# Optimization experiments

Hardware: AMD Instinct MI355X
Metric: run time of the kernel (lower is better)

The kernel has to match this reference:

```python
import jax, jax.numpy as jnp
import numpy as np

B, DIM, HEADS, H, W = 4, 64, 8, 512, 512


def _conv(x, w, groups=1):
    # NCHW x, OIHW w, stride 1, SAME padding (padding=k//2 in torch)
    return jax.lax.conv_general_dilated(
        x, w, (1, 1), 'SAME', feature_group_count=groups,
        dimension_numbers=('NCHW', 'OIHW', 'NCHW'))


def _dwt_haar(x):
    # single-level orthonormal haar on even-sized NCHW input
    a = x[..., 0::2, 0::2]; b = x[..., 0::2, 1::2]
    c = x[..., 1::2, 0::2]; d = x[..., 1::2, 1::2]
    LL = (a + b + c + d) * 0.5
    LH = (-a - b + c + d) * 0.5
    HL = (-a + b - c + d) * 0.5
    HH = (a - b - c + d) * 0.5
    return LL, LH, HL, HH


def _idwt_haar(LL, LH, HL, HH):
    a = (LL - LH - HL + HH) * 0.5
    b = (LL - LH + HL - HH) * 0.5
    c = (LL + LH - HL - HH) * 0.5
    d = (LL + LH + HL + HH) * 0.5
    Bn, C, h, w = LL.shape
    even = jnp.stack([a, b], -1).reshape(Bn, C, h, 2 * w)  # rows 0::2
    odd = jnp.stack([c, d], -1).reshape(Bn, C, h, 2 * w)   # rows 1::2
    return jnp.stack([even, odd], -2).reshape(Bn, C, 2 * h, 2 * w)


def _l2norm(x, eps=1e-12):
    n = jnp.sqrt(jnp.sum(x * x, axis=-1, keepdims=True))
    return x / jnp.maximum(n, eps)


def setup_inputs() -> dict:
    key = jax.random.key(0)
    ks = jax.random.split(key, 8)
    def w(k, shape):
        fan_in = shape[1] * shape[2] * shape[3]
        return jax.random.normal(k, shape, jnp.float32) * (1.0 / np.sqrt(fan_in))
    return {
        'x': jax.random.normal(ks[0], (B, DIM, H, W), jnp.float32),
        'w_hc1': w(ks[1], (2 * DIM, DIM, 3, 3)),        # groups=2 over 2*dim channels
        'w_hc2': w(ks[2], (DIM, 2 * DIM, 1, 1)),
        'w_ho': w(ks[3], (3 * DIM, DIM, 3, 3)),          # groups=3 over 3*dim channels
        'w_qkv': w(ks[4], (3 * DIM, DIM, 1, 1)),
        'w_dw': w(ks[5], (3 * DIM, 1, 3, 3)),            # depthwise, groups=3*dim
        'w_proj': w(ks[6], (DIM, DIM, 1, 1)),
        'temperature': jnp.ones((HEADS, 1, 1), jnp.float32),
    }


def reference(x, w_hc1, w_hc2, w_ho, w_qkv, w_dw, w_proj, temperature):
    LL, LH, HL, HH = _dwt_haar(x)

    # high-frequency (LH,HL) filter branch
    hv = jnp.concatenate([LH, HL], axis=1)
    filter_hv = jax.nn.relu(_conv(jax.nn.relu(_conv(hv, w_hc1, groups=2)), w_hc2))

    # qkv from LL: 1x1 conv then depthwise 3x3
    qkv = _conv(_conv(LL, w_qkv), w_dw, groups=3 * DIM)
    q, k, v = jnp.split(qkv, 3, axis=1)
    b, c, h, w = q.shape
    v = v * filter_hv + v

    ch = c // HEADS
    q = q.reshape(b, HEADS, ch, h * w)
    k = k.reshape(b, HEADS, ch, h * w)
    v = v.reshape(b, HEADS, ch, h * w)
    q = _l2norm(q)
    k = _l2norm(k)

    attn = jnp.einsum('bhcn,bhdn->bhcd', q, k) * temperature  # [b,heads,ch,ch]
    attn = jax.nn.softmax(attn, axis=-1)
    out = jnp.einsum('bhcd,bhdn->bhcn', attn, v).reshape(b, c, h, w)
    out = _conv(out, w_proj)

    # high-frequency output branch
    yh = jax.nn.relu(_conv(jnp.concatenate([LH, HL, HH], axis=1), w_ho, groups=3))
    LH2, HL2, HH2 = jnp.split(yh, 3, axis=1)

    return _idwt_haar(out, LH2, HL2, HH2)
```

## Files before the change

### kernel.cpp

```cpp
#include <hip/hip_runtime.h>
#include <hip/hip_bf16.h>

#define BN 4
#define DIM 64
#define NHEADS 8
#define HH 256
#define WH 256
#define NP (HH*WH)
#define HF 512
#define WF 512

#define PD 258
#define PROW (PD*64)
#define PPLANE ((size_t)PD*PD*64)

typedef __attribute__((ext_vector_type(8))) short bfx8;
typedef __attribute__((ext_vector_type(8))) unsigned short u16x8;
typedef __attribute__((ext_vector_type(4))) unsigned short u16x4;
typedef __attribute__((ext_vector_type(4))) float f32x4;

static __device__ __forceinline__ short f2bf(float f) {
    unsigned u = __float_as_uint(f);
    unsigned r = (u + 0x7FFFu + ((u >> 16) & 1u)) >> 16;
    return (short)r;
}
static __device__ __forceinline__ float bfu(unsigned short u) {
    return __uint_as_float((unsigned)u << 16);
}

__global__ __launch_bounds__(256) void k_setup(unsigned short* __restrict__ tiled16,
                                               const float* __restrict__ w_ho,
                                               const float* __restrict__ w_hc1,
                                               const float* __restrict__ w_hc2,
                                               const float* __restrict__ w_qkv,
                                               short* __restrict__ wrHO,
                                               short* __restrict__ wrHC1,
                                               short* __restrict__ wrHC2,
                                               short* __restrict__ wrQKV) {
    int bx = blockIdx.x, tid = threadIdx.x;
    if (bx < 16) {
        char* base = (char*)(tiled16 + (size_t)bx * PPLANE);
        const int ROWB = PROW * 2;
        for (int k = tid; k < 8224; k += 256) {
            char* dst;
            if (k < 2064) dst = base + (size_t)k * 16;
            else if (k < 4128) dst = base + (size_t)257 * ROWB + (size_t)(k - 2064) * 16;
            else if (k < 6176) { int r = (k - 4128) >> 3, s = (k - 4128) & 7;
                dst = base + (size_t)(r + 1) * ROWB + (size_t)s * 16; }
            else { int r = (k - 6176) >> 3, s = (k - 6176) & 7;
                dst = base + (size_t)(r + 1) * ROWB + 257 * 128 + (size_t)s * 16; }
            *(uint4*)dst = (uint4){0, 0, 0, 0};
        }
        return;
    }
    if (bx < 16 + 432 + 288) {
        const float* w = (bx < 448) ? w_ho : w_hc1;
        short* wrep = (bx < 448) ? wrHO : wrHC1;
        int t = (bx - ((bx < 448) ? 16 : 448)) * 256 + tid;
        unsigned g   = (unsigned)t / 36864u;
        unsigned r1  = (unsigned)t % 36864u;
        unsigned tap = r1 / 4096u;
        unsigned r2  = r1 % 4096u;
        unsigned icb = r2 / 512u;
        unsigned r3  = r2 % 512u;
        unsigned oc  = r3 >> 3;
        unsigned j   = r3 & 7u;
        wrep[t] = f2bf(w[(((size_t)g * 64 + oc) * 64 + icb * 8u + j) * 9 + tap]);
        return;
    }
    if (bx < 16 + 432 + 288 + 32) {
        int t = (bx - 736) * 256 + tid;
        int j = t & 7, gr = t >> 3, o16 = gr & 15, X = gr >> 4;
        int icb = X % 16, oct = X / 16;
        wrHC2[t] = f2bf(w_hc2[(size_t)(oct * 16 + o16) * 128 + icb * 8 + j]);
        return;
    }
    {
        int t = (bx - 768) * 256 + tid;
        int j = t & 7, gr = t >> 3, o16 = gr & 15, X = gr >> 4;
        int icb = X % 8, oct = X / 8;
        wrQKV[t] = f2bf(w_qkv[(size_t)(oct * 16 + o16) * 64 + icb * 8 + j]);
    }
}

__global__ __launch_bounds__(256) void k_dwt(const float* __restrict__ x,
                                             unsigned short* __restrict__ tiled,
                                             unsigned short* __restrict__ llp) {
    __shared__ unsigned short lds[3 * 128 * 64] __attribute__((aligned(16)));
    const int tid = threadIdx.x;
    const int pid = blockIdx.x;
    const int b = blockIdx.y;
    const int y0 = (pid >> 4) * 8, x0 = (pid & 15) * 16;
    const int quad = tid & 127;
    const int qy = quad >> 4, qx = quad & 15;
    const int gy = y0 + qy, gx = x0 + qx;
    const int ich = tid >> 7;
    unsigned short* llb = llp + (size_t)b * PPLANE + ((size_t)(gy + 1) * PD + (gx + 1)) * 64;

#pragma unroll 4
    for (int it = 0; it < 16; ++it) {
        int ic = it * 4 + ich * 2;
        unsigned g = (((unsigned)(ic >> 3)) + (unsigned)gx + 2u * (unsigned)gy) & 7u;
        unsigned swz = (unsigned)quad * 64 + (g << 3) + (unsigned)(ic & 7);
        unsigned pk[3], pll;
#pragma unroll
        for (int s = 0; s < 2; ++s) {
            const float* px = x + (((size_t)(b * 64 + ic + s) * HF) + 2 * gy) * WF + 2 * gx;
            float2 e0 = *(const float2*)px;
            float2 e1 = *(const float2*)(px + WF);
            float a = e0.x, bb = e0.y, c = e1.x, d = e1.y;
            unsigned ll = (unsigned short)f2bf(( a + bb + c + d) * 0.5f);
            unsigned lh = (unsigned short)f2bf((-a - bb + c + d) * 0.5f);
            unsigned hl = (unsigned short)f2bf((-a + bb - c + d) * 0.5f);
            unsigned hh = (unsigned short)f2bf(( a - bb - c + d) * 0.5f);
            if (s == 0) { pll = ll; pk[0] = lh; pk[1] = hl; pk[2] = hh; }
            else { pll |= ll << 16; pk[0] |= lh << 16; pk[1] |= hl << 16; pk[2] |= hh << 16; }
        }
        *(unsigned*)&lds[swz]          = pk[0];
        *(unsigned*)&lds[8192 + swz]   = pk[1];
        *(unsigned*)&lds[16384 + swz]  = pk[2];
        *(unsigned*)&llb[(g << 3) + (unsigned)(ic & 7)] = pll;
    }
    __syncthreads();
#pragma unroll
    for (int it = 0; it < 12; ++it) {
        int cch = tid + it * 256;
        int p = cch >> 10, rem = cch & 1023;
        int row = rem >> 7, col = rem & 127;
        unsigned short* dst = tiled + ((size_t)(b * 3 + p) * PD + (y0 + row + 1)) * PROW
                                    + (size_t)(x0 + 1) * 64 + (size_t)col * 8;
        *(uint4*)dst = *(const uint4*)((const char*)lds + (size_t)cch * 16);
    }
}

template <int LAYOUT>
__global__ __launch_bounds__(256) void k_gconv3x3_mfma(const unsigned short* __restrict__ tiled,
                                                       const bfx8* __restrict__ wr,
                                                       unsigned short* __restrict__ out, int OC) {
    __shared__ short lds_in[324 * 64] __attribute__((aligned(16)));
    const int tid = threadIdx.x;
    const int l = tid & 63, wv = tid >> 6;
    const int tile = blockIdx.x;
    const int x0 = (tile & 15) * 16, y0 = (tile >> 4) * 16;
    const int g = blockIdx.y, b = blockIdx.z;
    const unsigned short* src = tiled + (size_t)(b * 3 + g) * PPLANE;

#pragma unroll
    for (int it = 0; it < 10; ++it) {
        int cch = it * 256 + tid;
        unsigned row = (unsigned)cch / 144u, col = (unsigned)cch % 144u;
        const unsigned short* ga = src + (size_t)(y0 + row) * PROW + (size_t)x0 * 64 + (size_t)col * 8;
        __builtin_amdgcn_global_load_lds(
            (const __attribute__((address_space(1))) void*)ga,
            (__attribute__((address_space(3))) void*)((char*)lds_in + (size_t)(it * 256 + wv * 64) * 16),
            16, 0, 0);
    }
    if (tid < 32) {
        int cch = 2560 + tid;
        unsigned row = (unsigned)cch / 144u, col = (unsigned)cch % 144u;
        const unsigned short* ga = src + (size_t)(y0 + row) * PROW + (size_t)x0 * 64 + (size_t)col * 8;
        *(uint4*)((char*)lds_in + (size_t)cch * 16) = *(const uint4*)ga;
    }
    __syncthreads();

    f32x4 acc[4][4];
#pragma unroll
    for (int i = 0; i < 4; ++i)
#pragma unroll
        for (int j = 0; j < 4; ++j) acc[i][j] = (f32x4){0.f, 0.f, 0.f, 0.f};

    const int lx = l & 15, lq = l >> 4;
#pragma unroll
    for (int c = 0; c < 2; ++c) {
        const int icb = c * 4 + lq;
#pragma unroll
        for (int tap = 0; tap < 9; ++tap) {
            const int dy = tap / 3, dx = tap % 3;
            const size_t wbase = ((size_t)(g * 9 + tap) * 8 + icb) * 64 + lx;
            bfx8 b0 = wr[wbase];
            bfx8 b1 = wr[wbase + 16];
            bfx8 b2 = wr[wbase + 32];
            bfx8 b3 = wr[wbase + 48];
#pragma unroll
            for (int pg = 0; pg < 4; ++pg) {
                int hy = wv * 4 + pg + dy, hx = lx + dx;
                int hp = hy * 18 + hx;
                const bfx8* ap = (const bfx8*)&lds_in[hp * 64 + (((icb + hx + 2 * hy + 5) & 7) << 3)];
                bfx8 a = *ap;
                acc[pg][0] = __builtin_amdgcn_mfma_f32_16x16x32_bf16(a, b0, acc[pg][0], 0, 0, 0);
                acc[pg][1] = __builtin_amdgcn_mfma_f32_16x16x32_bf16(a, b1, acc[pg][1], 0, 0, 0);
                acc[pg][2] = __builtin_amdgcn_mfma_f32_16x16x32_bf16(a, b2, acc[pg][2], 0, 0, 0);
                acc[pg][3] = __builtin_amdgcn_mfma_f32_16x16x32_bf16(a, b3, acc[pg][3], 0, 0, 0);
            }
        }
    }

#pragma unroll
    for (int pg = 0; pg < 4; ++pg) {
#pragma unroll
        for (int ocg = 0; ocg < 4; ++ocg) {
            f32x4 v = acc[pg][ocg];
            if (LAYOUT == 0) {
                unsigned short* op = out + ((size_t)(b * 256 + tile) * OC + g * 64 + ocg * 16 + lx) * 256
                                         + (wv * 4 + pg) * 16 + lq * 4;
                ushort4 s4;
                s4.x = (unsigned short)f2bf(fmaxf(v.x, 0.f));
                s4.y = (unsigned short)f2bf(fmaxf(v.y, 0.f));
                s4.z = (unsigned short)f2bf(fmaxf(v.z, 0.f));
                s4.w = (unsigned short)f2bf(fmaxf(v.w, 0.f));
                *(ushort4*)op = s4;
            } else {
                int icT = g * 64 + ocg * 16 + lx;
                int g16 = icT >> 3;
                unsigned short* tb = out + ((size_t)(b * 256 + tile) * 256) * 128;
                int innerb = (wv * 4 + pg) * 16 + lq * 4;
                float vr[4] = {v.x, v.y, v.z, v.w};
#pragma unroll
                for (int r = 0; r < 4; ++r) {
                    int inn = innerb + r;
                    tb[(size_t)inn * 128 + (((g16 + inn) & 15) << 3) + (icT & 7)] =
                        (unsigned short)f2bf(fmaxf(vr[r], 0.f));
                }
            }
        }
    }
}

template <int CIN, int OC, bool RELU>
__global__ __launch_bounds__(256) void k_conv1x1_mfma(const unsigned short* __restrict__ inT,
                                                      const bfx8* __restrict__ wr,
                                                      unsigned short* __restrict__ out) {
    constexpr int KB = CIN / 8;
    constexpr int KC = CIN / 32;
    constexpr int NOCT = OC / 16;
    __shared__ short ldsA[256 * CIN] __attribute__((aligned(16)));
    const int tid = threadIdx.x;
    const int l = tid & 63, wv = tid >> 6;
    const int tile = blockIdx.x, b = blockIdx.y;
    const unsigned short* src = inT + ((size_t)(b * 256 + tile) * 256) * CIN;
    constexpr int ITER = (256 * CIN / 8) / 256;
#pragma unroll
    for (int it = 0; it < ITER; ++it) {
        int cc = it * 256 + tid;
        __builtin_amdgcn_global_load_lds(
            (const __attribute__((address_space(1))) void*)(src + (size_t)cc * 8),
            (__attribute__((address_space(3))) void*)((char*)ldsA + (size_t)(it * 256 + wv * 64) * 16),
            16, 0, 0);
    }
    __syncthreads();

    const int lx = l & 15, lq = l >> 4;
#pragma unroll
    for (int o4 = 0; o4 < NOCT / 4; ++o4) {
        f32x4 acc[4][4];
#pragma unroll
        for (int i = 0; i < 4; ++i)
#pragma unroll
            for (int j = 0; j < 4; ++j) acc[i][j] = (f32x4){0.f, 0.f, 0.f, 0.f};
#pragma unroll
        for (int c = 0; c < KC; ++c) {
            const int icb = c * 4 + lq;
            bfx8 bf[4];
#pragma unroll
            for (int ot = 0; ot < 4; ++ot)
                bf[ot] = wr[(size_t)(((o4 * 4 + ot) * KB + icb) * 16) + lx];
#pragma unroll
            for (int pg = 0; pg < 4; ++pg) {
                int inner = (wv * 4 + pg) * 16 + lx;
                const bfx8* ap = (const bfx8*)&ldsA[inner * CIN + (((icb + inner) & (KB - 1)) << 3)];
                bfx8 a = *ap;
                acc[pg][0] = __builtin_amdgcn_mfma_f32_16x16x32_bf16(a, bf[0], acc[pg][0], 0, 0, 0);
                acc[pg][1] = __builtin_amdgcn_mfma_f32_16x16x32_bf16(a, bf[1], acc[pg][1], 0, 0, 0);
                acc[pg][2] = __builtin_amdgcn_mfma_f32_16x16x32_bf16(a, bf[2], acc[pg][2], 0, 0, 0);
                acc[pg][3] = __builtin_amdgcn_mfma_f32_16x16x32_bf16(a, bf[3], acc[pg][3], 0, 0, 0);
            }
        }
#pragma unroll
        for (int pg = 0; pg < 4; ++pg)
#pragma unroll
            for (int ot = 0; ot < 4; ++ot) {
                int oc = (o4 * 4 + ot) * 16 + lx;
                unsigned short* op = out + ((size_t)(b * 256 + tile) * OC + oc) * 256
                                         + (wv * 4 + pg) * 16 + lq * 4;
                f32x4 v = acc[pg][ot];
                ushort4 s4;
                s4.x = (unsigned short)f2bf(RELU ? fmaxf(v.x, 0.f) : v.x);
                s4.y = (unsigned short)f2bf(RELU ? fmaxf(v.y, 0.f) : v.y);
                s4.z = (unsigned short)f2bf(RELU ? fmaxf(v.z, 0.f) : v.z);
                s4.w = (unsigned short)f2bf(RELU ? fmaxf(v.w, 0.f) : v.w);
                *(ushort4*)op = s4;
            }
    }
}

__global__ __launch_bounds__(256) void k_qkv_fused(const unsigned short* __restrict__ llp,
                                                   const bfx8* __restrict__ wrq,
                                                   const float* __restrict__ wdw,
                                                   const unsigned short* __restrict__ filt,
                                                   unsigned short* __restrict__ vt,
                                                   float* __restrict__ praw,
                                                   float* __restrict__ praw2) {
    __shared__ short ldsA[336 * 64] __attribute__((aligned(16)));
    __shared__ short qsave[64 * 256] __attribute__((aligned(16)));
    __shared__ float ssq[2][4][64];
    const int tid = threadIdx.x;
    const int l = tid & 63, wv = tid >> 6;
    const int tile = blockIdx.x, b = blockIdx.y;
    const int x0 = (tile & 15) * 16, y0 = (tile >> 4) * 16;
    const unsigned short* src = llp + (size_t)b * PPLANE;

#pragma unroll
    for (int it = 0; it < 10; ++it) {
        int cch = it * 256 + tid;
        unsigned row = (unsigned)cch / 144u, col = (unsigned)cch % 144u;
        const unsigned short* ga = src + (size_t)(y0 + row) * PROW + (size_t)x0 * 64 + (size_t)col * 8;
        __builtin_amdgcn_global_load_lds(
            (const __attribute__((address_space(1))) void*)ga,
            (__attribute__((address_space(3))) void*)((char*)ldsA + (size_t)(it * 256 + wv * 64) * 16),
            16, 0, 0);
    }
    if (tid < 32) {
        int cch = 2560 + tid;
        unsigned row = (unsigned)cch / 144u, col = (unsigned)cch % 144u;
        const unsigned short* ga = src + (size_t)(y0 + row) * PROW + (size_t)x0 * 64 + (size_t)col * 8;
        *(uint4*)((char*)ldsA + (size_t)cch * 16) = *(const uint4*)ga;
    }
    __syncthreads();

    const int lx = l & 15, lq = l >> 4;
    bfx8 af[6][2];
#pragma unroll
    for (int m = 0; m < 6; ++m) {
        int mt = wv + 4 * m;
        if (mt < 21) {
            int hp = mt * 16 + lx;
            int hy = hp / 18, hx = hp - hy * 18;
#pragma unroll
            for (int kc = 0; kc < 2; ++kc) {
                int icb = kc * 4 + lq;
                af[m][kc] = *(const bfx8*)&ldsA[hp * 64 + (((icb + hx + 2 * hy + 5) & 7) << 3)];
            }
        }
    }
    __syncthreads();

    for (int g3 = 0; g3 < 3; ++g3) {
        bfx8 bw[2][4];
#pragma unroll
        for (int kc = 0; kc < 2; ++kc)
#pragma unroll
            for (int nt = 0; nt < 4; ++nt)
                bw[kc][nt] = wrq[(size_t)(((g3 * 4 + nt) * 8) + kc * 4 + lq) * 16 + lx];
#pragma unroll
        for (int m = 0; m < 6; ++m) {
            int mt = wv + 4 * m;
            if (mt < 21) {
                f32x4 acc[4];
#pragma unroll
                for (int nt = 0; nt < 4; ++nt) acc[nt] = (f32x4){0.f, 0.f, 0.f, 0.f};
#pragma unroll
                for (int kc = 0; kc < 2; ++kc) {
                    bfx8 a = af[m][kc];
#pragma unroll
                    for (int nt = 0; nt < 4; ++nt)
                        acc[nt] = __builtin_amdgcn_mfma_f32_16x16x32_bf16(a, bw[kc][nt], acc[nt], 0, 0, 0);
                }
#pragma unroll
                for (int nt = 0; nt < 4; ++nt) {
                    int ocl = nt * 16 + lx;
                    float vr[4] = {acc[nt].x, acc[nt].y, acc[nt].z, acc[nt].w};
#pragma unroll
                    for (int r = 0; r < 4; ++r) {
                        int hp2 = mt * 16 + lq * 4 + r;
                        int hy2 = hp2 / 18, hx2 = hp2 - hy2 * 18;
                        ldsA[hp2 * 64 + ((((ocl >> 3) + hx2 + 2 * hy2) & 7) << 3) + (ocl & 7)] =
                            f2bf(vr[r]);
                    }
                }
            }
        }
        __syncthreads();
        const int ch = l, chg = g3 * 64 + ch;
        float w9[9];
#pragma unroll
        for (int t = 0; t < 9; ++t) w9[t] = wdw[chg * 9 + t];
        float s2 = 0.f;
        u16x8 kpk[4][2];
#pragma unroll
        for (int yy = 0; yy < 4; ++yy) {
            int y = wv * 4 + yy;
            float ln[3][18];
#pragma unroll
            for (int hr = 0; hr < 3; ++hr) {
                int hy = y + hr;
#pragma unroll
                for (int hx = 0; hx < 18; ++hx)
                    ln[hr][hx] = bfu((unsigned short)ldsA[(hy * 18 + hx) * 64 +
                                     ((((ch >> 3) + hx + 2 * hy) & 7) << 3) + (ch & 7)]);
            }
            float ox[16];
#pragma unroll
            for (int xx = 0; xx < 16; ++xx) {
                float s = 0.f;
#pragma unroll
                for (int hr = 0; hr < 3; ++hr)
#pragma unroll
                    for (int dx = 0; dx < 3; ++dx)
                        s = fmaf(ln[hr][xx + dx], w9[hr * 3 + dx], s);
                ox[xx] = s;
            }
            if (g3 == 2) {
                const unsigned short* fp = filt + ((size_t)(b * 256 + tile) * 64 + ch) * 256 + y * 16;
                u16x8 f0 = *(const u16x8*)fp;
                u16x8 f1 = *(const u16x8*)(fp + 8);
#pragma unroll
                for (int k = 0; k < 8; ++k) ox[k]     = fmaf(ox[k],     bfu(f0[k]), ox[k]);
#pragma unroll
                for (int k = 0; k < 8; ++k) ox[8 + k] = fmaf(ox[8 + k], bfu(f1[k]), ox[8 + k]);
                unsigned short* vb = vt + ((size_t)(b * 256 + tile) * 256 + (size_t)y * 16) * 64 + ch;
#pragma unroll
                for (int xx = 0; xx < 16; ++xx) vb[xx * 64] = (unsigned short)f2bf(ox[xx]);
            } else {
#pragma unroll
                for (int xx = 0; xx < 16; ++xx) s2 = fmaf(ox[xx], ox[xx], s2);
                if (g3 == 0) {
#pragma unroll
                    for (int xx = 0; xx < 16; ++xx) {
                        int px = y * 16 + xx;
                        qsave[ch * 256 + ((((px >> 3) + ch) & 31) << 3) + (px & 7)] =
                            f2bf(ox[xx]);
                    }
                } else {
#pragma unroll
                    for (int xx = 0; xx < 8; ++xx)  kpk[yy][0][xx] = (unsigned short)f2bf(ox[xx]);
#pragma unroll
                    for (int xx = 0; xx < 8; ++xx)  kpk[yy][1][xx] = (unsigned short)f2bf(ox[8 + xx]);
                }
            }
        }
        if (g3 == 0) ssq[0][wv][ch] = s2;
        if (g3 == 1) {
            ssq[1][wv][ch] = s2;
            __syncthreads();
            short* kbuf = ldsA;
#pragma unroll
            for (int yy = 0; yy < 4; ++yy) {
                int y = wv * 4 + yy;
#pragma unroll
                for (int xx = 0; xx < 16; ++xx) {
                    int px = y * 16 + xx;
                    kbuf[ch * 256 + ((((px >> 3) + ch) & 31) << 3) + (px & 7)] =
                        (short)kpk[yy][xx >> 3][xx & 7];
                }
            }
            __syncthreads();
            f32x4 sacc[4];
#pragma unroll
            for (int t16 = 0; t16 < 4; ++t16) sacc[t16] = (f32x4){0.f, 0.f, 0.f, 0.f};
#pragma unroll
            for (int kc2 = 0; kc2 < 2; ++kc2) {
                int kc = wv * 2 + kc2;
#pragma unroll
                for (int t16 = 0; t16 < 4; ++t16) {
                    int chh = t16 * 16 + lx;
                    int go = chh * 256 + (((kc * 4 + lq + chh) & 31) << 3);
                    bfx8 aq = *(const bfx8*)&qsave[go];
                    bfx8 bk = *(const bfx8*)&kbuf[go];
                    sacc[t16] = __builtin_amdgcn_mfma_f32_16x16x32_bf16(aq, bk, sacc[t16], 0, 0, 0);
                }
            }
            __syncthreads();
            float* sred = (float*)qsave;
#pragma unroll
            for (int t16 = 0; t16 < 4; ++t16)
                *(f32x4*)&sred[((wv * 4 + t16) * 64 + l) * 4] = sacc[t16];
            __syncthreads();
            {
                int t16r = tid >> 6, lr = tid & 63;
                f32x4 s0 = *(const f32x4*)&sred[((0 * 4 + t16r) * 64 + lr) * 4];
                f32x4 s1 = *(const f32x4*)&sred[((1 * 4 + t16r) * 64 + lr) * 4];
                f32x4 s2r = *(const f32x4*)&sred[((2 * 4 + t16r) * 64 + lr) * 4];
                f32x4 s3 = *(const f32x4*)&sred[((3 * 4 + t16r) * 64 + lr) * 4];
                f32x4 sum = s0 + s1 + s2r + s3;
                *(f32x4*)&praw[(((size_t)(b * 256 + tile) * 4 + t16r) * 64 + lr) * 4] = sum;
                if (tid < 128) {
                    int which = tid >> 6, chh = tid & 63;
                    praw2[(size_t)(b * 256 + tile) * 128 + tid] =
                        ssq[which][0][chh] + ssq[which][1][chh] +
                        ssq[which][2][chh] + ssq[which][3][chh];
                }
            }
        }
        __syncthreads();
    }
}

__global__ __launch_bounds__(512) void k_soft_prep(const float* __restrict__ praw,
                                                   const float* __restrict__ praw2,
                                                   const float* __restrict__ temp,
                                                   const float* __restrict__ wproj,
                                                   short* __restrict__ mrep) {
    __shared__ float sm[512];
    __shared__ float ash[512];
    const int b = blockIdx.x, tid = threadIdx.x;
    const int hd = tid >> 6, t = tid & 63;
    const int c = t >> 3, d = t & 7;
    const int t16 = hd >> 1, half = hd & 1;
    const int cl = half * 8 + c, dl = half * 8 + d;
    const float* pb = praw + ((size_t)(b * 256) * 4 + t16) * 256 + ((cl >> 2) * 16 + dl) * 4 + (cl & 3);
    const float* p2 = praw2 + (size_t)(b * 256) * 128;
    float s = 0.f, sq = 0.f, sk = 0.f;
    for (int tile = 0; tile < 256; ++tile) {
        s  += pb[(size_t)tile * 1024];
        sq += p2[(size_t)tile * 128 + hd * 8 + c];
        sk += p2[(size_t)tile * 128 + 64 + hd * 8 + d];
    }
    float nq = fmaxf(sqrtf(sq), 1e-12f);
    float nk = fmaxf(sqrtf(sk), 1e-12f);
    s = s / (nq * nk) * temp[hd];
    sm[tid] = s;
    __syncthreads();
    float mx = -1e30f;
#pragma unroll
    for (int dd = 0; dd < 8; ++dd) mx = fmaxf(mx, sm[hd * 64 + c * 8 + dd]);
    float e = __expf(s - mx);
    ash[tid] = e;
    __syncthreads();
    float sum = 0.f;
#pragma unroll
    for (int dd = 0; dd < 8; ++dd) sum += ash[hd * 64 + c * 8 + dd];
    float a = e / sum;
    __syncthreads();
    ash[tid] = a;
    __syncthreads();
#pragma unroll
    for (int i = 0; i < 8; ++i) {
        int idx = tid * 8 + i;
        int j = idx & 7, o16 = (idx >> 3) & 15, icb = (idx >> 7) & 7, oct = idx >> 10;
        int oc = oct * 16 + o16;
        float m = 0.f;
#pragma unroll
        for (int c8 = 0; c8 < 8; ++c8)
            m = fmaf(wproj[(size_t)oc * 64 + icb * 8 + c8], ash[icb * 64 + c8 * 8 + j], m);
        mrep[(size_t)b * 4096 + idx] = f2bf(m);
    }
}

__global__ __launch_bounds__(256) void k_attnout_idwt(const unsigned short* __restrict__ vt,
                                                      const bfx8* __restrict__ mrep,
                                                      const unsigned short* __restrict__ yht,
                                                      float* __restrict__ out) {
    const int tid = threadIdx.x;
    const int l = tid & 63, wv = tid >> 6;
    const int lx = l & 15, lq = l >> 4;
    const int tile = blockIdx.x, b = blockIdx.y;
    const int x0 = (tile & 15) * 16, y0 = (tile >> 4) * 16;
    const bfx8* vtb = (const bfx8*)(vt + (size_t)(b * 256 + tile) * 256 * 64);
    const bfx8* mb = mrep + (size_t)b * 512;

    bfx8 bw[2][4];
#pragma unroll
    for (int kc = 0; kc < 2; ++kc)
#pragma unroll
        for (int nt = 0; nt < 4; ++nt)
            bw[kc][nt] = mb[(nt * 8 + kc * 4 + lq) * 16 + lx];

    const unsigned short* yb = yht + (size_t)(b * 256 + tile) * 192 * 256;

#pragma unroll
    for (int pg = 0; pg < 4; ++pg) {
        const int mt = wv * 4 + pg;
        const int y = y0 + mt;
        bfx8 a0 = vtb[(mt * 16 + lx) * 8 + lq];
        bfx8 a1 = vtb[(mt * 16 + lx) * 8 + 4 + lq];

        f32x4 acc[4];
#pragma unroll
        for (int nt = 0; nt < 4; ++nt) acc[nt] = (f32x4){0.f, 0.f, 0.f, 0.f};
#pragma unroll
        for (int nt = 0; nt < 4; ++nt) {
            acc[nt] = __builtin_amdgcn_mfma_f32_16x16x32_bf16(a0, bw[0][nt], acc[nt], 0, 0, 0);
            acc[nt] = __builtin_amdgcn_mfma_f32_16x16x32_bf16(a1, bw[1][nt], acc[nt], 0, 0, 0);
        }
#pragma unroll
        for (int nt = 0; nt < 4; ++nt) {
            const int oc = nt * 16 + lx;
            const int inner = mt * 16 + lq * 4;
            const unsigned short* yp = yb + (size_t)oc * 256 + inner;
            u16x4 lh4 = *(const u16x4*)yp;
            u16x4 hl4 = *(const u16x4*)(yp + (size_t)64 * 256);
            u16x4 hh4 = *(const u16x4*)(yp + (size_t)128 * 256);
            float e0[8], e1[8];
#pragma unroll
            for (int r = 0; r < 4; ++r) {
                float s  = acc[nt][r];
                float LH = bfu(lh4[r]), HL = bfu(hl4[r]), HHv = bfu(hh4[r]);
                e0[2 * r]     = (s - LH - HL + HHv) * 0.5f;
                e0[2 * r + 1] = (s - LH + HL - HHv) * 0.5f;
                e1[2 * r]     = (s + LH - HL - HHv) * 0.5f;
                e1[2 * r + 1] = (s + LH + HL + HHv) * 0.5f;
            }
            float* o0 = out + ((size_t)(b * 64 + oc) * HF + 2 * y) * WF + 2 * (x0 + lq * 4);
            *(float4*)o0            = *(float4*)&e0[0];
            *(float4*)(o0 + 4)      = *(float4*)&e0[4];
            *(float4*)(o0 + WF)     = *(float4*)&e1[0];
            *(float4*)(o0 + WF + 4) = *(float4*)&e1[4];
        }
    }
}

extern "C" void kernel_launch(void* const* d_in, const int* in_sizes, int n_in,
                              void* d_out, int out_size, void* d_ws, size_t ws_size,
                              hipStream_t stream) {
    const float* x      = (const float*)d_in[0];
    const float* w_hc1  = (const float*)d_in[1];
    const float* w_hc2  = (const float*)d_in[2];
    const float* w_ho   = (const float*)d_in[3];
    const float* w_qkv  = (const float*)d_in[4];
    const float* w_dw   = (const float*)d_in[5];
    const float* w_proj = (const float*)d_in[6];
    const float* temp   = (const float*)d_in[7];
    float* out = (float*)d_out;

    char* base = (char*)d_ws;
    unsigned short* TILED = (unsigned short*)(base + 0);
    unsigned short* LLP   = (unsigned short*)(base + 102242304ULL);
    unsigned short* YH    = (unsigned short*)(base + 136323072ULL);
    unsigned short* T1T   = (unsigned short*)(base + 236986368ULL);
    unsigned short* FILT  = (unsigned short*)(base + 304095232ULL);
    unsigned short* VT    = (unsigned short*)(base + 337649664ULL);
    float*          PRAW  = (float*)(base + 371204096ULL);
    float*          PRAW2 = (float*)(base + 375398400ULL);
    short* WREP_HO  = (short*)(base + 375922688ULL);
    short* WREP_HC1 = (short*)(base + 376143872ULL);
    short* WREP_HC2 = (short*)(base + 376291328ULL);
    short* WREP_QKV = (short*)(base + 376307712ULL);
    short* MREP     = (short*)(base + 376332288ULL);

    k_setup<<<816, 256, 0, stream>>>(TILED, w_ho, w_hc1, w_hc2, w_qkv,
                                     WREP_HO, WREP_HC1, WREP_HC2, WREP_QKV);
    k_dwt<<<dim3(512, BN), 256, 0, stream>>>(x, TILED, LLP);
    k_gconv3x3_mfma<0><<<dim3(256, 3, BN), 256, 0, stream>>>(TILED, (const bfx8*)WREP_HO, YH, 192);
    k_gconv3x3_mfma<1><<<dim3(256, 2, BN), 256, 0, stream>>>(TILED, (const bfx8*)WREP_HC1, T1T, 128);
    k_conv1x1_mfma<128, 64, true><<<dim3(256, BN), 256, 0, stream>>>(T1T, (const bfx8*)WREP_HC2, FILT);
    k_qkv_fused<<<dim3(256, BN), 256, 0, stream>>>(LLP, (const bfx8*)WREP_QKV, w_dw, FILT,
                                                   VT, PRAW, PRAW2);
    k_soft_prep<<<BN, 512, 0, stream>>>(PRAW, PRAW2, temp, w_proj, MREP);
    k_attnout_idwt<<<dim3(256, BN), 256, 0, stream>>>(VT, (const bfx8*)MREP, YH, out);
}
```

Measured before the change: 559.2 us.

## Halve qkv tile height to 8 rows to cut LDS and raise occupancy

The fused qkv kernel now processes 16x8 tiles instead of 16x16, doubling the grid and halving LDS for the halo buffer and q save area. The per-tile partial Gram and norm buffers double in count, and the softmax prep kernel reduces over 512 partials instead of 256. The goal is more resident blocks per CU and better latency hiding. In exchange, the 3x3 halo grows relative to the useful area, so recomputation rises, and the serial reduction in k_soft_prep gets longer.

```diff
diff --git a/kernel.cpp b/kernel.cpp
--- a/kernel.cpp
+++ b/kernel.cpp
@@ -300,17 +300,20 @@
                                                    unsigned short* __restrict__ vt,
                                                    float* __restrict__ praw,
                                                    float* __restrict__ praw2) {
-    __shared__ short ldsA[336 * 64] __attribute__((aligned(16)));
-    __shared__ short qsave[64 * 256] __attribute__((aligned(16)));
+    __shared__ short ldsA[192 * 64] __attribute__((aligned(16)));
+    __shared__ short qsave[64 * 128] __attribute__((aligned(16)));
     __shared__ float ssq[2][4][64];
     const int tid = threadIdx.x;
     const int l = tid & 63, wv = tid >> 6;
-    const int tile = blockIdx.x, b = blockIdx.y;
-    const int x0 = (tile & 15) * 16, y0 = (tile >> 4) * 16;
+    const int st = blockIdx.x, b = blockIdx.y;
+    const int sy = st >> 4, sx = st & 15;
+    const int y0 = sy * 8, x0 = sx * 16;
+    const int tile16 = (sy >> 1) * 16 + sx;
+    const int yoff16 = (sy & 1) * 8;
     const unsigned short* src = llp + (size_t)b * PPLANE;
 
 #pragma unroll
-    for (int it = 0; it < 10; ++it) {
+    for (int it = 0; it < 5; ++it) {
         int cch = it * 256 + tid;
         unsigned row = (unsigned)cch / 144u, col = (unsigned)cch % 144u;
         const unsigned short* ga = src + (size_t)(y0 + row) * PROW + (size_t)x0 * 64 + (size_t)col * 8;
@@ -319,8 +322,8 @@
             (__attribute__((address_space(3))) void*)((char*)ldsA + (size_t)(it * 256 + wv * 64) * 16),
             16, 0, 0);
     }
-    if (tid < 32) {
-        int cch = 2560 + tid;
+    if (tid < 160) {
+        int cch = 1280 + tid;
         unsigned row = (unsigned)cch / 144u, col = (unsigned)cch % 144u;
         const unsigned short* ga = src + (size_t)(y0 + row) * PROW + (size_t)x0 * 64 + (size_t)col * 8;
         *(uint4*)((char*)ldsA + (size_t)cch * 16) = *(const uint4*)ga;
@@ -328,18 +331,16 @@
     __syncthreads();
 
     const int lx = l & 15, lq = l >> 4;
-    bfx8 af[6][2];
-#pragma unroll
-    for (int m = 0; m < 6; ++m) {
+    bfx8 af[3][2];
+#pragma unroll
+    for (int m = 0; m < 3; ++m) {
         int mt = wv + 4 * m;
-        if (mt < 21) {
-            int hp = mt * 16 + lx;
-            int hy = hp / 18, hx = hp - hy * 18;
-#pragma unroll
-            for (int kc = 0; kc < 2; ++kc) {
-                int icb = kc * 4 + lq;
-                af[m][kc] = *(const bfx8*)&ldsA[hp * 64 + (((icb + hx + 2 * hy + 5) & 7) << 3)];
-            }
+        int hp = mt * 16 + lx;
+        int hy = hp / 18, hx = hp - hy * 18;
+#pragma unroll
+        for (int kc = 0; kc < 2; ++kc) {
+            int icb = kc * 4 + lq;
+            af[m][kc] = *(const bfx8*)&ldsA[hp * 64 + (((icb + hx + 2 * hy + 5) & 7) << 3)];
         }
     }
     __syncthreads();
@@ -352,30 +353,28 @@
             for (int nt = 0; nt < 4; ++nt)
                 bw[kc][nt] = wrq[(size_t)(((g3 * 4 + nt) * 8) + kc * 4 + lq) * 16 + lx];
 #pragma unroll
-        for (int m = 0; m < 6; ++m) {
+        for (int m = 0; m < 3; ++m) {
             int mt = wv + 4 * m;
-            if (mt < 21) {
-                f32x4 acc[4];
-#pragma unroll
-                for (int nt = 0; nt < 4; ++nt) acc[nt] = (f32x4){0.f, 0.f, 0.f, 0.f};
-#pragma unroll
-                for (int kc = 0; kc < 2; ++kc) {
-                    bfx8 a = af[m][kc];
-#pragma unroll
-                    for (int nt = 0; nt < 4; ++nt)
-                        acc[nt] = __builtin_amdgcn_mfma_f32_16x16x32_bf16(a, bw[kc][nt], acc[nt], 0, 0, 0);
-                }
-#pragma unroll
-                for (int nt = 0; nt < 4; ++nt) {
-                    int ocl = nt * 16 + lx;
-                    float vr[4] = {acc[nt].x, acc[nt].y, acc[nt].z, acc[nt].w};
-#pragma unroll
-                    for (int r = 0; r < 4; ++r) {
-                        int hp2 = mt * 16 + lq * 4 + r;
-                        int hy2 = hp2 / 18, hx2 = hp2 - hy2 * 18;
-                        ldsA[hp2 * 64 + ((((ocl >> 3) + hx2 + 2 * hy2) & 7) << 3) + (ocl & 7)] =
-                            f2bf(vr[r]);
-                    }
+            f32x4 acc[4];
+#pragma unroll
+            for (int nt = 0; nt < 4; ++nt) acc[nt] = (f32x4){0.f, 0.f, 0.f, 0.f};
+#pragma unroll
+            for (int kc = 0; kc < 2; ++kc) {
+                bfx8 a = af[m][kc];
+#pragma unroll
+                for (int nt = 0; nt < 4; ++nt)
+                    acc[nt] = __builtin_amdgcn_mfma_f32_16x16x32_bf16(a, bw[kc][nt], acc[nt], 0, 0, 0);
+            }
+#pragma unroll
+            for (int nt = 0; nt < 4; ++nt) {
+                int ocl = nt * 16 + lx;
+                float vr[4] = {acc[nt].x, acc[nt].y, acc[nt].z, acc[nt].w};
+#pragma unroll
+                for (int r = 0; r < 4; ++r) {
+                    int hp2 = mt * 16 + lq * 4 + r;
+                    int hy2 = hp2 / 18, hx2 = hp2 - hy2 * 18;
+                    ldsA[hp2 * 64 + ((((ocl >> 3) + hx2 + 2 * hy2) & 7) << 3) + (ocl & 7)] =
+                        f2bf(vr[r]);
                 }
             }
         }
@@ -385,10 +384,10 @@
 #pragma unroll
         for (int t = 0; t < 9; ++t) w9[t] = wdw[chg * 9 + t];
         float s2 = 0.f;
-        u16x8 kpk[4][2];
-#pragma unroll
-        for (int yy = 0; yy < 4; ++yy) {
-            int y = wv * 4 + yy;
+        u16x8 kpk[2][2];
+#pragma unroll
+        for (int yy = 0; yy < 2; ++yy) {
+            int y = wv * 2 + yy;
             float ln[3][18];
 #pragma unroll
             for (int hr = 0; hr < 3; ++hr) {
@@ -410,14 +409,16 @@
                 ox[xx] = s;
             }
             if (g3 == 2) {
-                const unsigned short* fp = filt + ((size_t)(b * 256 + tile) * 64 + ch) * 256 + y * 16;
+                const unsigned short* fp = filt + ((size_t)(b * 256 + tile16) * 64 + ch) * 256
+                                               + (yoff16 + y) * 16;
                 u16x8 f0 = *(const u16x8*)fp;
                 u16x8 f1 = *(const u16x8*)(fp + 8);
 #pragma unroll
                 for (int k = 0; k < 8; ++k) ox[k]     = fmaf(ox[k],     bfu(f0[k]), ox[k]);
 #pragma unroll
                 for (int k = 0; k < 8; ++k) ox[8 + k] = fmaf(ox[8 + k], bfu(f1[k]), ox[8 + k]);
-                unsigned short* vb = vt + ((size_t)(b * 256 + tile) * 256 + (size_t)y * 16) * 64 + ch;
+                unsigned short* vb = vt + ((size_t)(b * 256 + tile16) * 256
+                                           + (size_t)(yoff16 + y) * 16) * 64 + ch;
 #pragma unroll
                 for (int xx = 0; xx < 16; ++xx) vb[xx * 64] = (unsigned short)f2bf(ox[xx]);
             } else {
@@ -427,7 +428,7 @@
 #pragma unroll
                     for (int xx = 0; xx < 16; ++xx) {
                         int px = y * 16 + xx;
-                        qsave[ch * 256 + ((((px >> 3) + ch) & 31) << 3) + (px & 7)] =
+                        qsave[ch * 128 + ((((px >> 3) + ch) & 15) << 3) + (px & 7)] =
                             f2bf(ox[xx]);
                     }
                 } else {
@@ -444,30 +445,26 @@
             __syncthreads();
             short* kbuf = ldsA;
 #pragma unroll
-            for (int yy = 0; yy < 4; ++yy) {
-                int y = wv * 4 + yy;
+            for (int yy = 0; yy < 2; ++yy) {
+                int y = wv * 2 + yy;
 #pragma unroll
                 for (int xx = 0; xx < 16; ++xx) {
                     int px = y * 16 + xx;
-                    kbuf[ch * 256 + ((((px >> 3) + ch) & 31) << 3) + (px & 7)] =
+                    kbuf[ch * 128 + ((((px >> 3) + ch) & 15) << 3) + (px & 7)] =
                         (short)kpk[yy][xx >> 3][xx & 7];
                 }
             }
             __syncthreads();
             f32x4 sacc[4];
-#pragma unroll
-            for (int t16 = 0; t16 < 4; ++t16) sacc[t16] = (f32x4){0.f, 0.f, 0.f, 0.f};
-#pragma unroll
-            for (int kc2 = 0; kc2 < 2; ++kc2) {
-                int kc = wv * 2 + kc2;
-#pragma unroll
-                for (int t16 = 0; t16 < 4; ++t16) {
-                    int chh = t16 * 16 + lx;
-                    int go = chh * 256 + (((kc * 4 + lq + chh) & 31) << 3);
-                    bfx8 aq = *(const bfx8*)&qsave[go];
-                    bfx8 bk = *(const bfx8*)&kbuf[go];
-                    sacc[t16] = __builtin_amdgcn_mfma_f32_16x16x32_bf16(aq, bk, sacc[t16], 0, 0, 0);
-                }
+            const int kc = wv;
+#pragma unroll
+            for (int t16 = 0; t16 < 4; ++t16) {
+                int chh = t16 * 16 + lx;
+                int go = chh * 128 + (((kc * 4 + lq + chh) & 15) << 3);
+                bfx8 aq = *(const bfx8*)&qsave[go];
+                bfx8 bk = *(const bfx8*)&kbuf[go];
+                sacc[t16] = __builtin_amdgcn_mfma_f32_16x16x32_bf16(
+                    aq, bk, (f32x4){0.f, 0.f, 0.f, 0.f}, 0, 0, 0);
             }
             __syncthreads();
             float* sred = (float*)qsave;
@@ -482,10 +479,10 @@
                 f32x4 s2r = *(const f32x4*)&sred[((2 * 4 + t16r) * 64 + lr) * 4];
                 f32x4 s3 = *(const f32x4*)&sred[((3 * 4 + t16r) * 64 + lr) * 4];
                 f32x4 sum = s0 + s1 + s2r + s3;
-                *(f32x4*)&praw[(((size_t)(b * 256 + tile) * 4 + t16r) * 64 + lr) * 4] = sum;
+                *(f32x4*)&praw[(((size_t)(b * 512 + st) * 4 + t16r) * 64 + lr) * 4] = sum;
                 if (tid < 128) {
                     int which = tid >> 6, chh = tid & 63;
-                    praw2[(size_t)(b * 256 + tile) * 128 + tid] =
+                    praw2[(size_t)(b * 512 + st) * 128 + tid] =
                         ssq[which][0][chh] + ssq[which][1][chh] +
                         ssq[which][2][chh] + ssq[which][3][chh];
                 }
@@ -507,10 +504,10 @@
     const int c = t >> 3, d = t & 7;
     const int t16 = hd >> 1, half = hd & 1;
     const int cl = half * 8 + c, dl = half * 8 + d;
-    const float* pb = praw + ((size_t)(b * 256) * 4 + t16) * 256 + ((cl >> 2) * 16 + dl) * 4 + (cl & 3);
-    const float* p2 = praw2 + (size_t)(b * 256) * 128;
+    const float* pb = praw + ((size_t)(b * 512) * 4 + t16) * 256 + ((cl >> 2) * 16 + dl) * 4 + (cl & 3);
+    const float* p2 = praw2 + (size_t)(b * 512) * 128;
     float s = 0.f, sq = 0.f, sk = 0.f;
-    for (int tile = 0; tile < 256; ++tile) {
+    for (int tile = 0; tile < 512; ++tile) {
         s  += pb[(size_t)tile * 1024];
         sq += p2[(size_t)tile * 128 + hd * 8 + c];
         sk += p2[(size_t)tile * 128 + 64 + hd * 8 + d];
@@ -630,12 +627,12 @@
     unsigned short* FILT  = (unsigned short*)(base + 304095232ULL);
     unsigned short* VT    = (unsigned short*)(base + 337649664ULL);
     float*          PRAW  = (float*)(base + 371204096ULL);
-    float*          PRAW2 = (float*)(base + 375398400ULL);
-    short* WREP_HO  = (short*)(base + 375922688ULL);
-    short* WREP_HC1 = (short*)(base + 376143872ULL);
-    short* WREP_HC2 = (short*)(base + 376291328ULL);
-    short* WREP_QKV = (short*)(base + 376307712ULL);
-    short* MREP     = (short*)(base + 376332288ULL);
+    float*          PRAW2 = (float*)(base + 379592704ULL);
+    short* WREP_HO  = (short*)(base + 380641280ULL);
+    short* WREP_HC1 = (short*)(base + 380862464ULL);
+    short* WREP_HC2 = (short*)(base + 381009920ULL);
+    short* WREP_QKV = (short*)(base + 381026304ULL);
+    short* MREP     = (short*)(base + 381050880ULL);
 
     k_setup<<<816, 256, 0, stream>>>(TILED, w_ho, w_hc1, w_hc2, w_qkv,
                                      WREP_HO, WREP_HC1, WREP_HC2, WREP_QKV);
@@ -643,7 +640,7 @@
     k_gconv3x3_mfma<0><<<dim3(256, 3, BN), 256, 0, stream>>>(TILED, (const bfx8*)WREP_HO, YH, 192);
     k_gconv3x3_mfma<1><<<dim3(256, 2, BN), 256, 0, stream>>>(TILED, (const bfx8*)WREP_HC1, T1T, 128);
     k_conv1x1_mfma<128, 64, true><<<dim3(256, BN), 256, 0, stream>>>(T1T, (const bfx8*)WREP_HC2, FILT);
-    k_qkv_fused<<<dim3(256, BN), 256, 0, stream>>>(LLP, (const bfx8*)WREP_QKV, w_dw, FILT,
+    k_qkv_fused<<<dim3(512, BN), 256, 0, stream>>>(LLP, (const bfx8*)WREP_QKV, w_dw, FILT,
                                                    VT, PRAW, PRAW2);
     k_soft_prep<<<BN, 512, 0, stream>>>(PRAW, PRAW2, temp, w_proj, MREP);
     k_attnout_idwt<<<dim3(256, BN), 256, 0, stream>>>(VT, (const bfx8*)MREP, YH, out);
```

Measured after the change: 577.7 us. 3.3% more time.
